# Kernel tuning notes

Hardware: AMD Instinct MI355X
Metric: run time of the kernel (lower is better)

Reference implementation:

```python
import jax, jax.numpy as jnp
import numpy as np

B, S, H = 8, 1024, 1024
NH, HD = 16, 64
MBANK, TOPK = 128, 16
NLAYERS, FF = 12, 4096
EPS = 1e-5


def _ln(x, w, b):
    m = x.mean(-1, keepdims=True)
    v = ((x - m) ** 2).mean(-1, keepdims=True)
    return (x - m) / jnp.sqrt(v + EPS) * w + b


def _split_heads(x):  # [B,S,H] -> [B,NH,S,HD]
    return x.reshape(B, S, NH, HD).transpose(0, 2, 1, 3)


def _sdpa(q, k, v):  # inputs [B,NH,S,HD]
    scores = jnp.einsum('bhqd,bhkd->bhqk', q, k) / jnp.sqrt(jnp.float32(HD))
    attn = jax.nn.softmax(scores, axis=-1)
    o = jnp.einsum('bhqk,bhkd->bhqd', attn, v)
    return o.transpose(0, 2, 1, 3).reshape(B, S, H)


def setup_inputs() -> dict:
    key = jax.random.key(0)
    ks = jax.random.split(key, 24)
    n = lambda k, shp, s=0.02: jax.random.normal(k, shp, jnp.float32) * s
    return {
        'hidden_states': jax.random.normal(ks[0], (B, S, H), jnp.float32),
        'ln1_w': jnp.ones((H,), jnp.float32), 'ln1_b': jnp.zeros((H,), jnp.float32),
        'ln2_w': jnp.ones((H,), jnp.float32), 'ln2_b': jnp.zeros((H,), jnp.float32),
        'rec_wq': n(ks[1], (H, H)), 'rec_wk': n(ks[2], (H, H)),
        'rec_wv': n(ks[3], (H, H)), 'rec_wo': n(ks[4], (H, H)),
        'rec_ad_w1': n(ks[5], (H // 4, H)), 'rec_ad_w2': n(ks[6], (H, H // 4)),
        'mem_bank': n(ks[7], (MBANK, H)),
        'alloc_w': n(ks[8], (MBANK, H)), 'alloc_b': jnp.zeros((MBANK,), jnp.float32),
        'retr_w': n(ks[9], (MBANK, H)), 'retr_b': jnp.zeros((MBANK,), jnp.float32),
        'upd_w': n(ks[10], (H, H)), 'upd_b': jnp.zeros((H,), jnp.float32),
        'mem_scales': jnp.full((NLAYERS,), 0.1, jnp.float32),
        'attn_in_w': n(ks[11], (3 * H, H)), 'attn_in_b': jnp.zeros((3 * H,), jnp.float32),
        'attn_out_w': n(ks[12], (H, H)), 'attn_out_b': jnp.zeros((H,), jnp.float32),
        'mlp_w1': n(ks[13], (FF, H)), 'mlp_b1': jnp.zeros((FF,), jnp.float32),
        'mlp_w2': n(ks[14], (H, FF)), 'mlp_b2': jnp.zeros((H,), jnp.float32),
        'layer_idx': 4,
    }


def reference(hidden_states, ln1_w, ln1_b, ln2_w, ln2_b,
              rec_wq, rec_wk, rec_wv, rec_wo, rec_ad_w1, rec_ad_w2,
              mem_bank, alloc_w, alloc_b, retr_w, retr_b, upd_w, upd_b, mem_scales,
              attn_in_w, attn_in_b, attn_out_w, attn_out_b,
              mlp_w1, mlp_b1, mlp_w2, mlp_b2, layer_idx):
    residual = hidden_states
    h = _ln(hidden_states, ln1_w, ln1_b)

    # --- CrossLayerParameterRecycler (layer_idx % 4 == 0 and > 0 -> recycle) ---
    if layer_idx % 4 == 0 and layer_idx > 0:
        q = _split_heads(h @ rec_wq.T)
        k = _split_heads(h @ rec_wk.T)
        v = _split_heads(h @ rec_wv.T)
        base_out = _sdpa(q, k, v) @ rec_wo.T
        h = jax.nn.relu(base_out @ rec_ad_w1.T) @ rec_ad_w2.T

    # --- CrossLayerMemoryManager ---
    pooled = h.mean(axis=1)                                  # [B,H]
    alloc_weights = jax.nn.softmax(pooled @ alloc_w.T + alloc_b, axis=-1)   # [B,MBANK]
    retr_weights = jax.nn.softmax(pooled @ retr_w.T + retr_b, axis=-1)
    retrieved = retr_weights @ mem_bank                      # [B,H]
    h = h + retrieved[:, None, :] * mem_scales[layer_idx]
    update_signals = jax.nn.sigmoid(h.mean(axis=1) @ upd_w.T + upd_b)       # [B,H]
    _, top_idx = jax.lax.top_k(alloc_weights, TOPK)          # [B,TOPK]

    # sequential per-batch scatter (later batches overwrite earlier, as in torch loop)
    def _write(mb, be):
        idx, sig = be
        return mb.at[idx].set(jnp.broadcast_to(sig, (TOPK, H))), None
    new_mem_bank, _ = jax.lax.scan(_write, mem_bank, (top_idx, update_signals))

    # --- self attention (nn.MultiheadAttention, batch_first) ---
    qkv = h @ attn_in_w.T + attn_in_b                        # [B,S,3H]
    q, k, v = jnp.split(qkv, 3, axis=-1)
    attn_out = _sdpa(_split_heads(q), _split_heads(k), _split_heads(v))
    attn_out = attn_out @ attn_out_w.T + attn_out_b
    h = residual + attn_out

    # --- MLP block ---
    residual2 = h
    h = _ln(h, ln2_w, ln2_b)
    h = jax.nn.gelu(h @ mlp_w1.T + mlp_b1, approximate=False) @ mlp_w2.T + mlp_b2
    out = residual2 + h
    return out, new_mem_bank
```

## Files before the change

### kernel.cpp

```cpp
#include <hip/hip_runtime.h>
#include <hip/hip_bf16.h>
#include <math.h>
#include <stdint.h>


#define BB 8
#define SS 1024
#define HH 1024
#define NHEAD 16
#define HD 64
#define MBANK 128
#define TOPK_N 16
#define FF_DIM 4096
#define MROWS (BB * SS)
#define NB_ELEM (8ull*1024*1024)

typedef __bf16 bf16x8 __attribute__((ext_vector_type(8)));
typedef __bf16 bf16x4 __attribute__((ext_vector_type(4)));
typedef float f32x4 __attribute__((ext_vector_type(4)));

#define SCALE_LOG2E 0.18033688011112042f

__device__ __forceinline__ unsigned short f2b(float x) {
  unsigned u = __float_as_uint(x);
  unsigned r = (u + 0x7FFFu + ((u >> 16) & 1u)) >> 16;
  return (unsigned short)r;
}
__device__ __forceinline__ float b2f(unsigned short u) {
  return __uint_as_float((unsigned)u << 16);
}

__device__ __forceinline__ float hmax4(f32x4 v) {
  return fmaxf(fmaxf(v[0], v[1]), fmaxf(v[2], v[3]));
}

__device__ __forceinline__ void load16_lds(const void* g, void* lds_base, int lane) {
#if __has_builtin(__builtin_amdgcn_global_load_lds)
  typedef const __attribute__((address_space(1))) unsigned int guint;
  typedef __attribute__((address_space(3))) unsigned int luint;
  __builtin_amdgcn_global_load_lds((guint*)(uintptr_t)g,
                                   (luint*)(unsigned long long)(unsigned int)(uintptr_t)lds_base,
                                   16, 0, 0);
#else
  *(uint4*)((char*)lds_base + lane * 16) = *(const uint4*)g;
#endif
}

__device__ __forceinline__ float gelu_exact(float x) {
  return 0.5f * x * (1.f + erff(x * 0.70710678118654752440f));
}


__global__ __launch_bounds__(256) void cast_split(const float* __restrict__ s,
                                                  unsigned short* __restrict__ hi,
                                                  unsigned short* __restrict__ lo, int n4) {
  int i = blockIdx.x * 256 + threadIdx.x;
  if (i < n4) {
    float4 v = ((const float4*)s)[i];
    ushort4 h, l;
    h.x = f2b(v.x); l.x = f2b(v.x - b2f(h.x));
    h.y = f2b(v.y); l.y = f2b(v.y - b2f(h.y));
    h.z = f2b(v.z); l.z = f2b(v.z - b2f(h.z));
    h.w = f2b(v.w); l.w = f2b(v.w - b2f(h.w));
    ((ushort4*)hi)[i] = h;
    ((ushort4*)lo)[i] = l;
  }
}

__global__ __launch_bounds__(256) void ln3(const float* __restrict__ x,
                                           const float* __restrict__ w,
                                           const float* __restrict__ b,
                                           unsigned short* __restrict__ yh,
                                           unsigned short* __restrict__ yl) {
  int row = blockIdx.x;
  const float* xr = x + (size_t)row * HH;
  int t = threadIdx.x;
  float v[4];
  float s = 0.f, ss = 0.f;
#pragma unroll
  for (int i = 0; i < 4; i++) {
    v[i] = xr[t + i * 256];
    s += v[i];
    ss += v[i] * v[i];
  }
  __shared__ float rs[8], rss[8];
  for (int o = 32; o > 0; o >>= 1) {
    s += __shfl_down(s, o, 64);
    ss += __shfl_down(ss, o, 64);
  }
  int wid = t >> 6, lane = t & 63;
  if (lane == 0) { rs[wid] = s; rss[wid] = ss; }
  __syncthreads();
  if (t == 0) {
    float S = rs[0] + rs[1] + rs[2] + rs[3];
    float SSum = rss[0] + rss[1] + rss[2] + rss[3];
    float m = S * (1.f / HH);
    float var = SSum * (1.f / HH) - m * m;
    rs[4] = m;
    rs[5] = rsqrtf(var + 1e-5f);
  }
  __syncthreads();
  float m = rs[4], inv = rs[5];
#pragma unroll
  for (int i = 0; i < 4; i++) {
    int c = t + i * 256;
    float y = (v[i] - m) * inv * w[c] + b[c];
    unsigned short h = f2b(y);
    yh[(size_t)row * HH + c] = h;
    yl[(size_t)row * HH + c] = f2b(y - b2f(h));
  }
}

template <int ACT, int MODE>
__global__ __launch_bounds__(256) void gemm3(const unsigned short* __restrict__ Ah,
                                             const unsigned short* __restrict__ Al, int lda,
                                             const unsigned short* __restrict__ Wh,
                                             const unsigned short* __restrict__ Wl, int ldw,
                                             unsigned short* __restrict__ Oh,
                                             unsigned short* __restrict__ Ol,
                                             float* __restrict__ outF,
                                             int ldo, int K) {
  __shared__ unsigned short Ash[2][128 * 32];
  __shared__ unsigned short Asl[2][128 * 32];
  __shared__ unsigned short Bsh[2][128 * 32];
  __shared__ unsigned short Bsl[2][128 * 32];
  int n0 = blockIdx.x * 128, m0 = blockIdx.y * 128;
  int t = threadIdx.x, w = t >> 6, L = t & 63, quad = L >> 4, l16 = L & 15;
  int wm = w & 1, wn = w >> 1;
  const f32x4 vzero = {0.f, 0.f, 0.f, 0.f};
  f32x4 acc[4][4];
#pragma unroll
  for (int i = 0; i < 4; i++)
#pragma unroll
    for (int j = 0; j < 4; j++) acc[i][j] = vzero;
  int srow = L >> 2;
  int scol = ((L & 3) ^ ((L >> 3) & 3)) * 8;
  int rsw = (l16 >> 1) & 3;

  auto stage = [&](int buf, int k0) {
#pragma unroll
    for (int c = 0; c < 2; c++) {
      int r = (c * 4 + w) * 16 + srow;
      size_t aoff = (size_t)(m0 + r) * lda + k0 + scol;
      size_t boff = (size_t)(n0 + r) * ldw + k0 + scol;
      load16_lds(Ah + aoff, &Ash[buf][(c * 4 + w) * 512], L);
      load16_lds(Al + aoff, &Asl[buf][(c * 4 + w) * 512], L);
      load16_lds(Wh + boff, &Bsh[buf][(c * 4 + w) * 512], L);
      load16_lds(Wl + boff, &Bsl[buf][(c * 4 + w) * 512], L);
    }
  };
  auto compute = [&](int buf) {
    bf16x8 afh[4], afl[4], bfh[4], bfl[4];
#pragma unroll
    for (int i = 0; i < 4; i++) {
      int off = (wm * 64 + i * 16 + l16) * 32 + (quad ^ rsw) * 8;
      afh[i] = *(const bf16x8*)&Ash[buf][off];
      afl[i] = *(const bf16x8*)&Asl[buf][off];
    }
#pragma unroll
    for (int j = 0; j < 4; j++) {
      int off = (wn * 64 + j * 16 + l16) * 32 + (quad ^ rsw) * 8;
      bfh[j] = *(const bf16x8*)&Bsh[buf][off];
      bfl[j] = *(const bf16x8*)&Bsl[buf][off];
    }
#pragma unroll
    for (int i = 0; i < 4; i++)
#pragma unroll
      for (int j = 0; j < 4; j++) {
        acc[i][j] = __builtin_amdgcn_mfma_f32_16x16x32_bf16(afh[i], bfh[j], acc[i][j], 0, 0, 0);
        acc[i][j] = __builtin_amdgcn_mfma_f32_16x16x32_bf16(afh[i], bfl[j], acc[i][j], 0, 0, 0);
        acc[i][j] = __builtin_amdgcn_mfma_f32_16x16x32_bf16(afl[i], bfh[j], acc[i][j], 0, 0, 0);
      }
  };

  stage(0, 0);
  __syncthreads();
  for (int k0 = 0; k0 < K; k0 += 64) {
    stage(1, k0 + 32);
    compute(0);
    __syncthreads();
    if (k0 + 64 < K) stage(0, k0 + 64);
    compute(1);
    __syncthreads();
  }
#pragma unroll
  for (int i = 0; i < 4; i++) {
    int mb = m0 + wm * 64 + i * 16 + quad * 4;
#pragma unroll
    for (int j = 0; j < 4; j++) {
      int n = n0 + wn * 64 + j * 16 + l16;
      if (MODE == 1) {
        ushort4 sh, sl;
        float vv[4];
#pragma unroll
        for (int r = 0; r < 4; r++) {
          float v = acc[i][j][r];
          if (ACT == 1) v = fmaxf(v, 0.f);
          vv[r] = v;
        }
        sh.x = f2b(vv[0]); sl.x = f2b(vv[0] - b2f(sh.x));
        sh.y = f2b(vv[1]); sl.y = f2b(vv[1] - b2f(sh.y));
        sh.z = f2b(vv[2]); sl.z = f2b(vv[2] - b2f(sh.z));
        sh.w = f2b(vv[3]); sl.w = f2b(vv[3] - b2f(sh.w));
        *(ushort4*)&Oh[(size_t)n * ldo + mb] = sh;
        *(ushort4*)&Ol[(size_t)n * ldo + mb] = sl;
      } else {
#pragma unroll
        for (int r = 0; r < 4; r++) {
          float v = acc[i][j][r];
          if (ACT == 1) v = fmaxf(v, 0.f);
          size_t off = (size_t)(mb + r) * ldo + n;
          if (MODE == 0) {
            unsigned short h = f2b(v);
            Oh[off] = h;
            Ol[off] = f2b(v - b2f(h));
          } else {
            outF[off] = v;
          }
        }
      }
    }
  }
}

__global__ __launch_bounds__(256) void sdpa3(const unsigned short* __restrict__ Qh,
                                             const unsigned short* __restrict__ Ql,
                                             const unsigned short* __restrict__ Kh,
                                             const unsigned short* __restrict__ Kl,
                                             const unsigned short* __restrict__ Vth,
                                             const unsigned short* __restrict__ Vtl,
                                             unsigned short* __restrict__ Oh,
                                             unsigned short* __restrict__ Ol) {
  __shared__ unsigned short Ksh[64 * 64];
  __shared__ unsigned short Ksl[64 * 64];
  __shared__ unsigned short Vsh[64 * 64];
  __shared__ unsigned short Vsl[64 * 64];
  int wg = (int)blockIdx.x;
  int swz = (wg & 7) * 256 + (wg >> 3);
  int qt = swz & 15, h = (swz >> 4) & 15, b = swz >> 8;
  int t = threadIdx.x, w = t >> 6, L = t & 63, quad = L >> 4, l16 = L & 15;
  int q0 = qt * 64;
  const f32x4 vzero = {0.f, 0.f, 0.f, 0.f};
  bf16x8 qfh[2], qfl[2];
  {
    size_t qrow = (size_t)(b * SS + q0 + w * 16 + l16);
#pragma unroll
    for (int kh = 0; kh < 2; kh++) {
      size_t off = qrow * HH + h * 64 + kh * 32 + quad * 8;
      qfh[kh] = *(const bf16x8*)&Qh[off];
      qfl[kh] = *(const bf16x8*)&Ql[off];
    }
  }
  float mprev = -1e30f, lsum = 0.f;
  f32x4 oacc[4];
#pragma unroll
  for (int jd = 0; jd < 4; jd++) oacc[jd] = vzero;
  int srow = L >> 3;
  int scolV = ((L & 7) ^ srow) * 8;
  int rbase = ((l16 & 12) << 1) | (l16 & 3);
  int keyK = (l16 & 3) | (((l16 >> 2) & 1) << 2);
  int k7 = l16 & 7;
  for (int k0 = 0; k0 < SS; k0 += 64) {
    __syncthreads();
#pragma unroll
    for (int c = 0; c < 2; c++) {
      int rr = (c * 4 + w) * 8 + srow;
      int scolK = ((L & 7) ^ ((srow & 3) | (((c * 4 + w) & 1) << 2))) * 8;
      size_t koff = (size_t)(b * SS + k0 + rr) * HH + h * 64 + scolK;
      size_t voff = (size_t)(h * 64 + rr) * MROWS + b * SS + k0 + scolV;
      load16_lds(Kh + koff, &Ksh[(c * 4 + w) * 512], L);
      load16_lds(Kl + koff, &Ksl[(c * 4 + w) * 512], L);
      load16_lds(Vth + voff, &Vsh[(c * 4 + w) * 512], L);
      load16_lds(Vtl + voff, &Vsl[(c * 4 + w) * 512], L);
    }
    __syncthreads();
    f32x4 sacc[4];
#pragma unroll
    for (int jn = 0; jn < 4; jn++) sacc[jn] = vzero;
#pragma unroll
    for (int jn = 0; jn < 4; jn++) {
      int rowp = rbase + (jn & 1) * 4 + (jn >> 1) * 32;
#pragma unroll
      for (int kh = 0; kh < 2; kh++) {
        int off = rowp * 64 + (((kh * 4 + quad) ^ keyK) << 3);
        bf16x8 kfh = *(const bf16x8*)&Ksh[off];
        bf16x8 kfl = *(const bf16x8*)&Ksl[off];
        sacc[jn] = __builtin_amdgcn_mfma_f32_16x16x32_bf16(kfh, qfh[kh], sacc[jn], 0, 0, 0);
        sacc[jn] = __builtin_amdgcn_mfma_f32_16x16x32_bf16(kfl, qfh[kh], sacc[jn], 0, 0, 0);
        sacc[jn] = __builtin_amdgcn_mfma_f32_16x16x32_bf16(kfh, qfl[kh], sacc[jn], 0, 0, 0);
      }
    }
    float mt = fmaxf(fmaxf(hmax4(sacc[0]), hmax4(sacc[1])),
                     fmaxf(hmax4(sacc[2]), hmax4(sacc[3])));
    mt = fmaxf(mt, __shfl_xor(mt, 16, 64));
    mt = fmaxf(mt, __shfl_xor(mt, 32, 64));
    float m2 = fmaxf(mprev, mt * SCALE_LOG2E);
    float rs = 0.f;
    bf16x8 pah[2], pal[2];
#pragma unroll
    for (int jn = 0; jn < 4; jn++) {
      int kh = jn >> 1, half = (jn & 1) * 4;
#pragma unroll
      for (int r = 0; r < 4; r++) {
        float p = exp2f(fmaf(sacc[jn][r], SCALE_LOG2E, -m2));
        rs += p;
        __bf16 ph = (__bf16)p;
        pah[kh][half + r] = ph;
        pal[kh][half + r] = (__bf16)(p - (float)ph);
      }
    }
    rs += __shfl_xor(rs, 16, 64);
    rs += __shfl_xor(rs, 32, 64);
    if (__any(m2 != mprev)) {
      float alpha = exp2f(mprev - m2);
      lsum = lsum * alpha + rs;
      float ar[4];
#pragma unroll
      for (int r = 0; r < 4; r++) ar[r] = __shfl(alpha, quad * 4 + r, 16);
#pragma unroll
      for (int jd = 0; jd < 4; jd++)
#pragma unroll
        for (int r = 0; r < 4; r++) oacc[jd][r] *= ar[r];
    } else {
      lsum += rs;
    }
    mprev = m2;
#pragma unroll
    for (int jd = 0; jd < 4; jd++)
#pragma unroll
      for (int kh = 0; kh < 2; kh++) {
        int off = (jd * 16 + l16) * 64 + ((kh * 4 + quad) ^ k7) * 8;
        bf16x8 vfh = *(const bf16x8*)&Vsh[off];
        bf16x8 vfl = *(const bf16x8*)&Vsl[off];
        oacc[jd] = __builtin_amdgcn_mfma_f32_16x16x32_bf16(pah[kh], vfh, oacc[jd], 0, 0, 0);
        oacc[jd] = __builtin_amdgcn_mfma_f32_16x16x32_bf16(pah[kh], vfl, oacc[jd], 0, 0, 0);
        oacc[jd] = __builtin_amdgcn_mfma_f32_16x16x32_bf16(pal[kh], vfh, oacc[jd], 0, 0, 0);
      }
  }
  float inv = 1.f / lsum;
  float invr[4];
#pragma unroll
  for (int r = 0; r < 4; r++) invr[r] = __shfl(inv, quad * 4 + r, 16);
#pragma unroll
  for (int r = 0; r < 4; r++) {
    size_t row = (size_t)(b * SS + q0 + w * 16 + quad * 4 + r);
#pragma unroll
    for (int jd = 0; jd < 4; jd++) {
      float v = oacc[jd][r] * invr[r];
      unsigned short hh = f2b(v);
      size_t off = row * HH + h * 64 + jd * 16 + l16;
      Oh[off] = hh;
      Ol[off] = f2b(v - b2f(hh));
    }
  }
}


__global__ __launch_bounds__(256) void meanpool_kernel(const float* __restrict__ Hb,
                                                       float* __restrict__ P) {
  int cb = blockIdx.x;
  int b = blockIdx.y;
  int t = threadIdx.x;
  int c = (t & 63) + cb * 64;
  int part = t >> 6;
  float s = 0.f;
  const float* p = Hb + ((size_t)b * SS + part * 256) * HH + c;
  for (int j = 0; j < 256; j++) s += p[(size_t)j * HH];
  __shared__ float red[4][64];
  red[part][t & 63] = s;
  __syncthreads();
  if (t < 64) {
    float tot = red[0][t] + red[1][t] + red[2][t] + red[3][t];
    P[b * HH + cb * 64 + t] = tot * (1.f / SS);
  }
}

__global__ __launch_bounds__(256) void memlogits_kernel(const float* __restrict__ P,
                                                        const float* __restrict__ AW,
                                                        const float* __restrict__ ABias,
                                                        const float* __restrict__ RW,
                                                        const float* __restrict__ RBias,
                                                        float* __restrict__ LA,
                                                        float* __restrict__ LR) {
  int m = blockIdx.x, b = blockIdx.y;
  int t = threadIdx.x;
  const float* pr = P + b * HH;
  const float* aw = AW + (size_t)m * HH;
  const float* rw = RW + (size_t)m * HH;
  float sa = 0.f, sr = 0.f;
  for (int i = t; i < HH; i += 256) {
    float pv = pr[i];
    sa = fmaf(pv, aw[i], sa);
    sr = fmaf(pv, rw[i], sr);
  }
  for (int o = 32; o > 0; o >>= 1) {
    sa += __shfl_down(sa, o, 64);
    sr += __shfl_down(sr, o, 64);
  }
  __shared__ float ra[4], rr[4];
  if ((t & 63) == 0) { ra[t >> 6] = sa; rr[t >> 6] = sr; }
  __syncthreads();
  if (t == 0) {
    LA[b * MBANK + m] = ra[0] + ra[1] + ra[2] + ra[3] + ABias[m];
    LR[b * MBANK + m] = rr[0] + rr[1] + rr[2] + rr[3] + RBias[m];
  }
}

__global__ __launch_bounds__(256) void retrieve_kernel(const float* __restrict__ LA,
                                                       const float* __restrict__ LR,
                                                       const float* __restrict__ MB,
                                                       float* __restrict__ RET,
                                                       int* __restrict__ ISTOP) {
  int b = blockIdx.x;
  int t = threadIdx.x;
  __shared__ float rw[MBANK];
  __shared__ float la[MBANK];
  if (t < MBANK) {
    la[t] = LA[b * MBANK + t];
    rw[t] = LR[b * MBANK + t];
  }
  __syncthreads();
  if (t == 0) {
    float mx = -1e30f;
    for (int i = 0; i < MBANK; i++) mx = fmaxf(mx, rw[i]);
    float s = 0.f;
    for (int i = 0; i < MBANK; i++) {
      float e = __expf(rw[i] - mx);
      rw[i] = e;
      s += e;
    }
    float inv = 1.f / s;
    for (int i = 0; i < MBANK; i++) rw[i] *= inv;
  }
  __syncthreads();
  if (t < MBANK) {
    float mine = la[t];
    int rank = 0;
    for (int i = 0; i < MBANK; i++) {
      float o = la[i];
      if (o > mine || (o == mine && i < t)) rank++;
    }
    ISTOP[b * MBANK + t] = (rank < TOPK_N) ? 1 : 0;
  }
  for (int c = t; c < HH; c += 256) {
    float s = 0.f;
    for (int m = 0; m < MBANK; m++) s = fmaf(rw[m], MB[(size_t)m * HH + c], s);
    RET[b * HH + c] = s;
  }
}

__global__ __launch_bounds__(256) void addmem_kernel(float* __restrict__ Hb,
                                                     const float* __restrict__ RET,
                                                     const float* __restrict__ scales,
                                                     const int* __restrict__ lidx) {
  float sc = scales[lidx[0]];
  size_t i = (size_t)blockIdx.x * 256 + threadIdx.x;
  int c = (int)(i & 1023);
  int b = (int)(i >> 20);
  Hb[i] = fmaf(RET[b * HH + c], sc, Hb[i]);
}

__global__ __launch_bounds__(256) void upd_kernel(const float* __restrict__ P2,
                                                  const float* __restrict__ UW,
                                                  const float* __restrict__ UB,
                                                  float* __restrict__ UPD) {
  int n = blockIdx.x, b = blockIdx.y;
  int t = threadIdx.x;
  const float* pr = P2 + b * HH;
  const float* wr = UW + (size_t)n * HH;
  float s = 0.f;
  for (int i = t; i < HH; i += 256) s = fmaf(pr[i], wr[i], s);
  for (int o = 32; o > 0; o >>= 1) s += __shfl_down(s, o, 64);
  __shared__ float red[4];
  if ((t & 63) == 0) red[t >> 6] = s;
  __syncthreads();
  if (t == 0) {
    float tot = red[0] + red[1] + red[2] + red[3] + UB[n];
    UPD[b * HH + n] = 1.f / (1.f + __expf(-tot));
  }
}

__global__ __launch_bounds__(256) void membank_kernel(const float* __restrict__ MB,
                                                      const int* __restrict__ ISTOP,
                                                      const float* __restrict__ UPD,
                                                      float* __restrict__ OUT) {
  int row = blockIdx.x;
  int col = blockIdx.y * 256 + threadIdx.x;
  int w = -1;
  for (int b = 0; b < BB; b++)
    if (ISTOP[b * MBANK + row]) w = b;
  float v = (w >= 0) ? UPD[w * HH + col] : MB[(size_t)row * HH + col];
  OUT[(size_t)row * HH + col] = v;
}


__global__ __launch_bounds__(256) void ln_bf(const float* __restrict__ x,
                                             const float* __restrict__ w,
                                             const float* __restrict__ b,
                                             unsigned short* __restrict__ y) {
  int row = blockIdx.x;
  const float* xr = x + (size_t)row * HH;
  unsigned short* yr = y + (size_t)row * HH;
  int t = threadIdx.x;
  float v[4];
  float s = 0.f, ss = 0.f;
#pragma unroll
  for (int i = 0; i < 4; i++) {
    v[i] = xr[t + i * 256];
    s += v[i];
    ss += v[i] * v[i];
  }
  __shared__ float rs[8], rss[8];
  for (int o = 32; o > 0; o >>= 1) {
    s += __shfl_down(s, o, 64);
    ss += __shfl_down(ss, o, 64);
  }
  int wid = t >> 6, lane = t & 63;
  if (lane == 0) { rs[wid] = s; rss[wid] = ss; }
  __syncthreads();
  if (t == 0) {
    float S = rs[0] + rs[1] + rs[2] + rs[3];
    float SSum = rss[0] + rss[1] + rss[2] + rss[3];
    float m = S * (1.f / HH);
    float var = SSum * (1.f / HH) - m * m;
    rs[4] = m;
    rs[5] = rsqrtf(var + 1e-5f);
  }
  __syncthreads();
  float m = rs[4], inv = rs[5];
#pragma unroll
  for (int i = 0; i < 4; i++) {
    int c = t + i * 256;
    yr[c] = f2b((v[i] - m) * inv * w[c] + b[c]);
  }
}

__global__ __launch_bounds__(256) void castf2b(const float* __restrict__ s,
                                               unsigned short* __restrict__ d, int n4) {
  int i = blockIdx.x * 256 + threadIdx.x;
  if (i < n4) {
    float4 v = ((const float4*)s)[i];
    ushort4 o;
    o.x = f2b(v.x); o.y = f2b(v.y); o.z = f2b(v.z); o.w = f2b(v.w);
    ((ushort4*)d)[i] = o;
  }
}

template <int ACT, int MODE>
__global__ __launch_bounds__(256) void gemm_bf(const unsigned short* __restrict__ A, int lda,
                                               const unsigned short* __restrict__ W, int ldw,
                                               const float* __restrict__ bias,
                                               const float* __restrict__ resid,
                                               float* __restrict__ outF,
                                               unsigned short* __restrict__ outB,
                                               int ldo, int K) {
  __shared__ unsigned short As[2][128 * 32];
  __shared__ unsigned short Bs[2][128 * 32];
  int n0 = blockIdx.x * 128, m0 = blockIdx.y * 128;
  int t = threadIdx.x, w = t >> 6, L = t & 63, quad = L >> 4, l16 = L & 15;
  int wm = w & 1, wn = w >> 1;
  const f32x4 vzero = {0.f, 0.f, 0.f, 0.f};
  f32x4 acc[4][4];
#pragma unroll
  for (int i = 0; i < 4; i++)
#pragma unroll
    for (int j = 0; j < 4; j++) acc[i][j] = vzero;
  int srow = L >> 2;
  int scol = ((L & 3) ^ ((L >> 3) & 3)) * 8;
  int rsw = (l16 >> 1) & 3;

  auto stage = [&](int buf, int k0) {
#pragma unroll
    for (int c = 0; c < 2; c++) {
      int r = (c * 4 + w) * 16 + srow;
      load16_lds(A + (size_t)(m0 + r) * lda + k0 + scol, &As[buf][(c * 4 + w) * 512], L);
      load16_lds(W + (size_t)(n0 + r) * ldw + k0 + scol, &Bs[buf][(c * 4 + w) * 512], L);
    }
  };
  auto compute = [&](int buf) {
    bf16x8 af[4], bfr[4];
#pragma unroll
    for (int i = 0; i < 4; i++)
      af[i] = *(const bf16x8*)&As[buf][(wm * 64 + i * 16 + l16) * 32 + (quad ^ rsw) * 8];
#pragma unroll
    for (int j = 0; j < 4; j++)
      bfr[j] = *(const bf16x8*)&Bs[buf][(wn * 64 + j * 16 + l16) * 32 + (quad ^ rsw) * 8];
#pragma unroll
    for (int i = 0; i < 4; i++)
#pragma unroll
      for (int j = 0; j < 4; j++)
        acc[i][j] = __builtin_amdgcn_mfma_f32_16x16x32_bf16(af[i], bfr[j], acc[i][j], 0, 0, 0);
  };

  stage(0, 0);
  __syncthreads();
  for (int k0 = 0; k0 < K; k0 += 64) {
    stage(1, k0 + 32);
    compute(0);
    __syncthreads();
    if (k0 + 64 < K) stage(0, k0 + 64);
    compute(1);
    __syncthreads();
  }
#pragma unroll
  for (int i = 0; i < 4; i++) {
    int mb = m0 + wm * 64 + i * 16 + quad * 4;
#pragma unroll
    for (int j = 0; j < 4; j++) {
      int n = n0 + wn * 64 + j * 16 + l16;
      float bv = bias ? bias[n] : 0.f;
      if (MODE == 2) {
        ushort4 st;
        float v0 = acc[i][j][0] + bv, v1 = acc[i][j][1] + bv;
        float v2 = acc[i][j][2] + bv, v3 = acc[i][j][3] + bv;
        if (ACT == 1) { v0 = fmaxf(v0, 0.f); v1 = fmaxf(v1, 0.f); v2 = fmaxf(v2, 0.f); v3 = fmaxf(v3, 0.f); }
        if (ACT == 2) { v0 = gelu_exact(v0); v1 = gelu_exact(v1); v2 = gelu_exact(v2); v3 = gelu_exact(v3); }
        st.x = f2b(v0); st.y = f2b(v1); st.z = f2b(v2); st.w = f2b(v3);
        *(ushort4*)&outB[(size_t)n * ldo + mb] = st;
      } else {
#pragma unroll
        for (int r = 0; r < 4; r++) {
          float v = acc[i][j][r] + bv;
          if (ACT == 1) v = fmaxf(v, 0.f);
          if (ACT == 2) v = gelu_exact(v);
          size_t off = (size_t)(mb + r) * ldo + n;
          if (MODE == 1) outB[off] = f2b(v);
          else if (MODE == 3) outF[off] += v;
          else if (MODE == 4) outF[off] = v + resid[off];
        }
      }
    }
  }
}

__global__ __launch_bounds__(256) void sdpa_bf(const unsigned short* __restrict__ Q,
                                               const unsigned short* __restrict__ Kb,
                                               const unsigned short* __restrict__ Vt,
                                               unsigned short* __restrict__ O) {
  __shared__ unsigned short Ks[64 * 64];
  __shared__ unsigned short Vs[64 * 64];
  int wg = (int)blockIdx.x;
  int swz = (wg & 7) * 256 + (wg >> 3);
  int qt = swz & 15, h = (swz >> 4) & 15, b = swz >> 8;
  int t = threadIdx.x, w = t >> 6, L = t & 63, quad = L >> 4, l16 = L & 15;
  int q0 = qt * 64;
  const f32x4 vzero = {0.f, 0.f, 0.f, 0.f};
  bf16x8 qf[2];
  {
    size_t qrow = (size_t)(b * SS + q0 + w * 16 + l16);
#pragma unroll
    for (int kh = 0; kh < 2; kh++)
      qf[kh] = *(const bf16x8*)&Q[qrow * HH + h * 64 + kh * 32 + quad * 8];
  }
  float mprev = -1e30f, lsum = 0.f;
  f32x4 oacc[4];
#pragma unroll
  for (int jd = 0; jd < 4; jd++) oacc[jd] = vzero;
  int srow = L >> 3;
  int scolV = ((L & 7) ^ srow) * 8;
  int rbase = ((l16 & 12) << 1) | (l16 & 3);
  int keyK = (l16 & 3) | (((l16 >> 2) & 1) << 2);
  int k7 = l16 & 7;
  for (int k0 = 0; k0 < SS; k0 += 64) {
    __syncthreads();
#pragma unroll
    for (int c = 0; c < 2; c++) {
      int rr = (c * 4 + w) * 8 + srow;
      int scolK = ((L & 7) ^ ((srow & 3) | (((c * 4 + w) & 1) << 2))) * 8;
      load16_lds(Kb + (size_t)(b * SS + k0 + rr) * HH + h * 64 + scolK, &Ks[(c * 4 + w) * 512], L);
      load16_lds(Vt + (size_t)(h * 64 + rr) * MROWS + b * SS + k0 + scolV, &Vs[(c * 4 + w) * 512], L);
    }
    __syncthreads();
    f32x4 sacc[4];
#pragma unroll
    for (int jn = 0; jn < 4; jn++) sacc[jn] = vzero;
#pragma unroll
    for (int jn = 0; jn < 4; jn++) {
      int rowp = rbase + (jn & 1) * 4 + (jn >> 1) * 32;
#pragma unroll
      for (int kh = 0; kh < 2; kh++) {
        bf16x8 kf = *(const bf16x8*)&Ks[rowp * 64 + (((kh * 4 + quad) ^ keyK) << 3)];
        sacc[jn] = __builtin_amdgcn_mfma_f32_16x16x32_bf16(kf, qf[kh], sacc[jn], 0, 0, 0);
      }
    }
    float mt = fmaxf(fmaxf(hmax4(sacc[0]), hmax4(sacc[1])),
                     fmaxf(hmax4(sacc[2]), hmax4(sacc[3])));
    mt = fmaxf(mt, __shfl_xor(mt, 16, 64));
    mt = fmaxf(mt, __shfl_xor(mt, 32, 64));
    float m2 = fmaxf(mprev, mt * SCALE_LOG2E);
    float rs = 0.f;
    bf16x8 pa[2];
#pragma unroll
    for (int jn = 0; jn < 4; jn++) {
      int kh = jn >> 1, half = (jn & 1) * 4;
#pragma unroll
      for (int r = 0; r < 4; r++) {
        float p = exp2f(fmaf(sacc[jn][r], SCALE_LOG2E, -m2));
        rs += p;
        pa[kh][half + r] = (__bf16)p;
      }
    }
    rs += __shfl_xor(rs, 16, 64);
    rs += __shfl_xor(rs, 32, 64);
    if (__any(m2 != mprev)) {
      float alpha = exp2f(mprev - m2);
      lsum = lsum * alpha + rs;
      float ar[4];
#pragma unroll
      for (int r = 0; r < 4; r++) ar[r] = __shfl(alpha, quad * 4 + r, 16);
#pragma unroll
      for (int jd = 0; jd < 4; jd++)
#pragma unroll
        for (int r = 0; r < 4; r++) oacc[jd][r] *= ar[r];
    } else {
      lsum += rs;
    }
    mprev = m2;
#pragma unroll
    for (int jd = 0; jd < 4; jd++)
#pragma unroll
      for (int kh = 0; kh < 2; kh++) {
        bf16x8 vf = *(const bf16x8*)&Vs[(jd * 16 + l16) * 64 + ((kh * 4 + quad) ^ k7) * 8];
        oacc[jd] = __builtin_amdgcn_mfma_f32_16x16x32_bf16(pa[kh], vf, oacc[jd], 0, 0, 0);
      }
  }
  float inv = 1.f / lsum;
  float invr[4];
#pragma unroll
  for (int r = 0; r < 4; r++) invr[r] = __shfl(inv, quad * 4 + r, 16);
#pragma unroll
  for (int r = 0; r < 4; r++) {
    size_t row = (size_t)(b * SS + q0 + w * 16 + quad * 4 + r);
#pragma unroll
    for (int jd = 0; jd < 4; jd++)
      O[row * HH + h * 64 + jd * 16 + l16] = f2b(oacc[jd][r] * invr[r]);
  }
}

extern "C" void kernel_launch(void* const* d_in, const int* in_sizes, int n_in,
                              void* d_out, int out_size, void* d_ws, size_t ws_size,
                              hipStream_t stream) {
  const float* x = (const float*)d_in[0];
  const float* ln1_w = (const float*)d_in[1];
  const float* ln1_b = (const float*)d_in[2];
  const float* ln2_w = (const float*)d_in[3];
  const float* ln2_b = (const float*)d_in[4];
  const float* rec_wq = (const float*)d_in[5];
  const float* rec_wk = (const float*)d_in[6];
  const float* rec_wv = (const float*)d_in[7];
  const float* rec_wo = (const float*)d_in[8];
  const float* rec_ad_w1 = (const float*)d_in[9];
  const float* rec_ad_w2 = (const float*)d_in[10];
  const float* mem_bank = (const float*)d_in[11];
  const float* alloc_w = (const float*)d_in[12];
  const float* alloc_b = (const float*)d_in[13];
  const float* retr_w = (const float*)d_in[14];
  const float* retr_b = (const float*)d_in[15];
  const float* upd_w = (const float*)d_in[16];
  const float* upd_b = (const float*)d_in[17];
  const float* mem_scales = (const float*)d_in[18];
  const float* attn_in_w = (const float*)d_in[19];
  const float* attn_in_b = (const float*)d_in[20];
  const float* attn_out_w = (const float*)d_in[21];
  const float* attn_out_b = (const float*)d_in[22];
  const float* mlp_w1 = (const float*)d_in[23];
  const float* mlp_b1 = (const float*)d_in[24];
  const float* mlp_w2 = (const float*)d_in[25];
  const float* mlp_b2 = (const float*)d_in[26];
  const int* layer_idx = (const int*)d_in[27];

  float* out = (float*)d_out;
  float* out_mb = out + NB_ELEM;

  const size_t U = NB_ELEM;
  unsigned short* W16 = (unsigned short*)d_ws;
  unsigned short* U0 = W16;
  unsigned short* U1 = W16 + U;
  unsigned short* U2 = W16 + 2 * U;
  unsigned short* U3 = W16 + 3 * U;
  unsigned short* U4 = W16 + 4 * U;
  unsigned short* U5 = W16 + 5 * U;
  unsigned short* wsh = W16 + 6 * U;
  unsigned short* wsl = wsh + 1048576;
  float* small = (float*)(wsl + 1048576);
  float* pooled = small;
  float* pooled2 = small + 8192;
  float* logitsA = small + 16384;
  float* logitsR = small + 17408;
  float* retrieved = small + 18432;
  float* updsig = small + 26624;
  int* istop = (int*)(small + 34816);
  unsigned short* D0 = (unsigned short*)out;
  unsigned short* D1 = D0 + U;
  unsigned short* ain_bf = U5;
  unsigned short* aout_bf = U5 + 3 * 1048576;

  dim3 blk(256);
  dim3 gG(8, 64);
  dim3 gG256(2, 64);
  dim3 gS1(2048);
  const int EW_GRID = (int)(NB_ELEM / 256);

  ln3<<<MROWS, blk, 0, stream>>>(x, ln1_w, ln1_b, U0, U1);
  cast_split<<<1024, blk, 0, stream>>>(rec_wq, wsh, wsl, 262144);
  gemm3<0, 0><<<gG, blk, 0, stream>>>(U0, U1, HH, wsh, wsl, HH, U2, U3, nullptr, HH, HH);
  cast_split<<<1024, blk, 0, stream>>>(rec_wk, wsh, wsl, 262144);
  gemm3<0, 0><<<gG, blk, 0, stream>>>(U0, U1, HH, wsh, wsl, HH, U4, U5, nullptr, HH, HH);
  cast_split<<<1024, blk, 0, stream>>>(rec_wv, wsh, wsl, 262144);
  gemm3<0, 1><<<gG, blk, 0, stream>>>(U0, U1, HH, wsh, wsl, HH, D0, D1, nullptr, MROWS, HH);
  sdpa3<<<gS1, blk, 0, stream>>>(U2, U3, U4, U5, D0, D1, U0, U1);
  cast_split<<<1024, blk, 0, stream>>>(rec_wo, wsh, wsl, 262144);
  gemm3<0, 0><<<gG, blk, 0, stream>>>(U0, U1, HH, wsh, wsl, HH, U2, U3, nullptr, HH, HH);
  cast_split<<<256, blk, 0, stream>>>(rec_ad_w1, wsh, wsl, 65536);
  gemm3<1, 0><<<gG256, blk, 0, stream>>>(U2, U3, HH, wsh, wsl, HH, U4, U4 + 2097152, nullptr, 256, HH);
  cast_split<<<256, blk, 0, stream>>>(rec_ad_w2, wsh, wsl, 65536);
  gemm3<0, 2><<<gG, blk, 0, stream>>>(U4, U4 + 2097152, 256, wsh, wsl, 256, nullptr, nullptr, out, HH, 256);
  meanpool_kernel<<<dim3(HH / 64, BB), blk, 0, stream>>>(out, pooled);
  memlogits_kernel<<<dim3(MBANK, BB), blk, 0, stream>>>(pooled, alloc_w, alloc_b, retr_w, retr_b, logitsA, logitsR);
  retrieve_kernel<<<BB, blk, 0, stream>>>(logitsA, logitsR, mem_bank, retrieved, istop);
  addmem_kernel<<<EW_GRID, blk, 0, stream>>>(out, retrieved, mem_scales, layer_idx);
  meanpool_kernel<<<dim3(HH / 64, BB), blk, 0, stream>>>(out, pooled2);
  upd_kernel<<<dim3(HH, BB), blk, 0, stream>>>(pooled2, upd_w, upd_b, updsig);
  membank_kernel<<<dim3(MBANK, HH / 256), blk, 0, stream>>>(mem_bank, istop, updsig, out_mb);
  castf2b<<<8192, blk, 0, stream>>>(out, U0, 2097152);
  castf2b<<<3072, blk, 0, stream>>>(attn_in_w, ain_bf, 786432);
  castf2b<<<1024, blk, 0, stream>>>(attn_out_w, aout_bf, 262144);
  gemm_bf<0, 1><<<gG, blk, 0, stream>>>(U0, HH, ain_bf, HH, attn_in_b, nullptr, nullptr, U1, HH, HH);
  gemm_bf<0, 1><<<gG, blk, 0, stream>>>(U0, HH, ain_bf + (size_t)HH * HH, HH, attn_in_b + HH, nullptr, nullptr, U2, HH, HH);
  gemm_bf<0, 2><<<gG, blk, 0, stream>>>(U0, HH, ain_bf + 2ull * HH * HH, HH, attn_in_b + 2 * HH, nullptr, nullptr, U3, MROWS, HH);
  sdpa_bf<<<gS1, blk, 0, stream>>>(U1, U2, U3, U4);
  gemm_bf<0, 4><<<gG, blk, 0, stream>>>(U4, HH, aout_bf, HH, attn_out_b, x, out, nullptr, HH, HH);
  ln_bf<<<MROWS, blk, 0, stream>>>(out, ln2_w, ln2_b, U1);
  {
    unsigned short* w1b = U0;
    unsigned short* w2b = U0 + 4 * 1048576;
    unsigned short* h2 = U2;
    castf2b<<<4096, blk, 0, stream>>>(mlp_w1, w1b, 1048576);
    castf2b<<<4096, blk, 0, stream>>>(mlp_w2, w2b, 1048576);
    gemm_bf<2, 1><<<dim3(32, 64), blk, 0, stream>>>(U1, HH, w1b, HH, mlp_b1, nullptr, nullptr, h2, FF_DIM, HH);
    gemm_bf<0, 3><<<gG, blk, 0, stream>>>(h2, FF_DIM, w2b, FF_DIM, mlp_b2, nullptr, out, nullptr, HH, FF_DIM);
  }
}
```

Before: 1.126 ms.

## Fuse memory-add into update and casts, merge cast launches, single-buffer gemm3

Removes the separate add-memory pass over the hidden states and the second mean-pool by folding the retrieved*scale term into the update GEMV and into the bf16 cast of the hidden states. Merges several weight-cast launches into combined kernels to cut launch count. It also changes gemm3 from double-buffered LDS staging to a single buffer with two barriers per 32-wide K step. That halves gemm3's LDS footprint but removes the load/compute overlap. The memory-add fusion relies on linearity of the mean, since pooled + ret*scale equals the mean of h + ret*scale.

```diff
diff --git a/kernel.cpp b/kernel.cpp
--- a/kernel.cpp
+++ b/kernel.cpp
@@ -16,7 +16,6 @@
 #define NB_ELEM (8ull*1024*1024)
 
 typedef __bf16 bf16x8 __attribute__((ext_vector_type(8)));
-typedef __bf16 bf16x4 __attribute__((ext_vector_type(4)));
 typedef float f32x4 __attribute__((ext_vector_type(4)));
 
 #define SCALE_LOG2E 0.18033688011112042f
@@ -67,6 +66,30 @@
   }
 }
 
+__global__ __launch_bounds__(256) void cast_split2(const float* __restrict__ s1,
+                                                   unsigned short* __restrict__ h1,
+                                                   unsigned short* __restrict__ l1, int n1,
+                                                   const float* __restrict__ s2,
+                                                   unsigned short* __restrict__ h2,
+                                                   unsigned short* __restrict__ l2, int n2) {
+  int i = blockIdx.x * 256 + threadIdx.x;
+  const float* s;
+  unsigned short* hh;
+  unsigned short* ll;
+  int j;
+  if (i < n1) { s = s1; hh = h1; ll = l1; j = i; }
+  else if (i < n1 + n2) { s = s2; hh = h2; ll = l2; j = i - n1; }
+  else return;
+  float4 v = ((const float4*)s)[j];
+  ushort4 h, l;
+  h.x = f2b(v.x); l.x = f2b(v.x - b2f(h.x));
+  h.y = f2b(v.y); l.y = f2b(v.y - b2f(h.y));
+  h.z = f2b(v.z); l.z = f2b(v.z - b2f(h.z));
+  h.w = f2b(v.w); l.w = f2b(v.w - b2f(h.w));
+  ((ushort4*)hh)[j] = h;
+  ((ushort4*)ll)[j] = l;
+}
+
 __global__ __launch_bounds__(256) void ln3(const float* __restrict__ x,
                                            const float* __restrict__ w,
                                            const float* __restrict__ b,
@@ -120,10 +143,10 @@
                                              unsigned short* __restrict__ Ol,
                                              float* __restrict__ outF,
                                              int ldo, int K) {
-  __shared__ unsigned short Ash[2][128 * 32];
-  __shared__ unsigned short Asl[2][128 * 32];
-  __shared__ unsigned short Bsh[2][128 * 32];
-  __shared__ unsigned short Bsl[2][128 * 32];
+  __shared__ unsigned short Ash[128 * 32];
+  __shared__ unsigned short Asl[128 * 32];
+  __shared__ unsigned short Bsh[128 * 32];
+  __shared__ unsigned short Bsl[128 * 32];
   int n0 = blockIdx.x * 128, m0 = blockIdx.y * 128;
   int t = threadIdx.x, w = t >> 6, L = t & 63, quad = L >> 4, l16 = L & 15;
   int wm = w & 1, wn = w >> 1;
@@ -136,32 +159,31 @@
   int srow = L >> 2;
   int scol = ((L & 3) ^ ((L >> 3) & 3)) * 8;
   int rsw = (l16 >> 1) & 3;
-
-  auto stage = [&](int buf, int k0) {
+  for (int k0 = 0; k0 < K; k0 += 32) {
+    __syncthreads();
 #pragma unroll
     for (int c = 0; c < 2; c++) {
       int r = (c * 4 + w) * 16 + srow;
       size_t aoff = (size_t)(m0 + r) * lda + k0 + scol;
       size_t boff = (size_t)(n0 + r) * ldw + k0 + scol;
-      load16_lds(Ah + aoff, &Ash[buf][(c * 4 + w) * 512], L);
-      load16_lds(Al + aoff, &Asl[buf][(c * 4 + w) * 512], L);
-      load16_lds(Wh + boff, &Bsh[buf][(c * 4 + w) * 512], L);
-      load16_lds(Wl + boff, &Bsl[buf][(c * 4 + w) * 512], L);
-    }
-  };
-  auto compute = [&](int buf) {
+      load16_lds(Ah + aoff, &Ash[(c * 4 + w) * 512], L);
+      load16_lds(Al + aoff, &Asl[(c * 4 + w) * 512], L);
+      load16_lds(Wh + boff, &Bsh[(c * 4 + w) * 512], L);
+      load16_lds(Wl + boff, &Bsl[(c * 4 + w) * 512], L);
+    }
+    __syncthreads();
     bf16x8 afh[4], afl[4], bfh[4], bfl[4];
 #pragma unroll
     for (int i = 0; i < 4; i++) {
       int off = (wm * 64 + i * 16 + l16) * 32 + (quad ^ rsw) * 8;
-      afh[i] = *(const bf16x8*)&Ash[buf][off];
-      afl[i] = *(const bf16x8*)&Asl[buf][off];
+      afh[i] = *(const bf16x8*)&Ash[off];
+      afl[i] = *(const bf16x8*)&Asl[off];
     }
 #pragma unroll
     for (int j = 0; j < 4; j++) {
       int off = (wn * 64 + j * 16 + l16) * 32 + (quad ^ rsw) * 8;
-      bfh[j] = *(const bf16x8*)&Bsh[buf][off];
-      bfl[j] = *(const bf16x8*)&Bsl[buf][off];
+      bfh[j] = *(const bf16x8*)&Bsh[off];
+      bfl[j] = *(const bf16x8*)&Bsl[off];
     }
 #pragma unroll
     for (int i = 0; i < 4; i++)
@@ -171,17 +193,6 @@
         acc[i][j] = __builtin_amdgcn_mfma_f32_16x16x32_bf16(afh[i], bfl[j], acc[i][j], 0, 0, 0);
         acc[i][j] = __builtin_amdgcn_mfma_f32_16x16x32_bf16(afl[i], bfh[j], acc[i][j], 0, 0, 0);
       }
-  };
-
-  stage(0, 0);
-  __syncthreads();
-  for (int k0 = 0; k0 < K; k0 += 64) {
-    stage(1, k0 + 32);
-    compute(0);
-    __syncthreads();
-    if (k0 + 64 < K) stage(0, k0 + 64);
-    compute(1);
-    __syncthreads();
   }
 #pragma unroll
   for (int i = 0; i < 4; i++) {
@@ -449,27 +460,24 @@
   }
 }
 
-__global__ __launch_bounds__(256) void addmem_kernel(float* __restrict__ Hb,
-                                                     const float* __restrict__ RET,
-                                                     const float* __restrict__ scales,
-                                                     const int* __restrict__ lidx) {
-  float sc = scales[lidx[0]];
-  size_t i = (size_t)blockIdx.x * 256 + threadIdx.x;
-  int c = (int)(i & 1023);
-  int b = (int)(i >> 20);
-  Hb[i] = fmaf(RET[b * HH + c], sc, Hb[i]);
-}
-
-__global__ __launch_bounds__(256) void upd_kernel(const float* __restrict__ P2,
+__global__ __launch_bounds__(256) void upd_kernel(const float* __restrict__ P,
+                                                  const float* __restrict__ RETR,
+                                                  const float* __restrict__ scales,
+                                                  const int* __restrict__ lidx,
                                                   const float* __restrict__ UW,
                                                   const float* __restrict__ UB,
                                                   float* __restrict__ UPD) {
   int n = blockIdx.x, b = blockIdx.y;
   int t = threadIdx.x;
-  const float* pr = P2 + b * HH;
+  float sc = scales[lidx[0]];
+  const float* pr = P + b * HH;
+  const float* rr2 = RETR + b * HH;
   const float* wr = UW + (size_t)n * HH;
   float s = 0.f;
-  for (int i = t; i < HH; i += 256) s = fmaf(pr[i], wr[i], s);
+  for (int i = t; i < HH; i += 256) {
+    float pv = fmaf(rr2[i], sc, pr[i]);
+    s = fmaf(pv, wr[i], s);
+  }
   for (int o = 32; o > 0; o >>= 1) s += __shfl_down(s, o, 64);
   __shared__ float red[4];
   if ((t & 63) == 0) red[t >> 6] = s;
@@ -535,15 +543,59 @@
   }
 }
 
-__global__ __launch_bounds__(256) void castf2b(const float* __restrict__ s,
-                                               unsigned short* __restrict__ d, int n4) {
+__global__ __launch_bounds__(256) void cast_attn_fused(const float* __restrict__ hs,
+                                                       const float* __restrict__ ret,
+                                                       const float* __restrict__ scales,
+                                                       const int* __restrict__ lidx,
+                                                       const float* __restrict__ ain_w,
+                                                       const float* __restrict__ aout_w,
+                                                       unsigned short* __restrict__ h_bf,
+                                                       unsigned short* __restrict__ ain_bf,
+                                                       unsigned short* __restrict__ aout_bf) {
   int i = blockIdx.x * 256 + threadIdx.x;
-  if (i < n4) {
-    float4 v = ((const float4*)s)[i];
+  if (i < 2097152) {
+    float sc = scales[lidx[0]];
+    float4 v = ((const float4*)hs)[i];
+    int e = i << 2;
+    int b = e >> 20;
+    int c = e & 1023;
+    float4 r4 = *(const float4*)&ret[b * HH + c];
+    ushort4 o;
+    o.x = f2b(fmaf(r4.x, sc, v.x));
+    o.y = f2b(fmaf(r4.y, sc, v.y));
+    o.z = f2b(fmaf(r4.z, sc, v.z));
+    o.w = f2b(fmaf(r4.w, sc, v.w));
+    ((ushort4*)h_bf)[i] = o;
+  } else if (i < 2097152 + 786432) {
+    int j = i - 2097152;
+    float4 v = ((const float4*)ain_w)[j];
     ushort4 o;
     o.x = f2b(v.x); o.y = f2b(v.y); o.z = f2b(v.z); o.w = f2b(v.w);
-    ((ushort4*)d)[i] = o;
-  }
+    ((ushort4*)ain_bf)[j] = o;
+  } else if (i < 2097152 + 786432 + 262144) {
+    int j = i - 2097152 - 786432;
+    float4 v = ((const float4*)aout_w)[j];
+    ushort4 o;
+    o.x = f2b(v.x); o.y = f2b(v.y); o.z = f2b(v.z); o.w = f2b(v.w);
+    ((ushort4*)aout_bf)[j] = o;
+  }
+}
+
+__global__ __launch_bounds__(256) void castf2b2(const float* __restrict__ s1,
+                                                unsigned short* __restrict__ d1, int n1,
+                                                const float* __restrict__ s2,
+                                                unsigned short* __restrict__ d2, int n2) {
+  int i = blockIdx.x * 256 + threadIdx.x;
+  const float* s;
+  unsigned short* d;
+  int j;
+  if (i < n1) { s = s1; d = d1; j = i; }
+  else if (i < n1 + n2) { s = s2; d = d2; j = i - n1; }
+  else return;
+  float4 v = ((const float4*)s)[j];
+  ushort4 o;
+  o.x = f2b(v.x); o.y = f2b(v.y); o.z = f2b(v.z); o.w = f2b(v.w);
+  ((ushort4*)d)[j] = o;
 }
 
 template <int ACT, int MODE>
@@ -784,7 +836,6 @@
   unsigned short* wsl = wsh + 1048576;
   float* small = (float*)(wsl + 1048576);
   float* pooled = small;
-  float* pooled2 = small + 8192;
   float* logitsA = small + 16384;
   float* logitsR = small + 17408;
   float* retrieved = small + 18432;
@@ -792,6 +843,12 @@
   int* istop = (int*)(small + 34816);
   unsigned short* D0 = (unsigned short*)out;
   unsigned short* D1 = D0 + U;
+  unsigned short* wkh = D0;
+  unsigned short* wkl = D0 + 1048576;
+  unsigned short* a1h = U0;
+  unsigned short* a1l = U0 + 262144;
+  unsigned short* a2h = U0 + 524288;
+  unsigned short* a2l = U0 + 786432;
   unsigned short* ain_bf = U5;
   unsigned short* aout_bf = U5 + 3 * 1048576;
 
@@ -799,32 +856,26 @@
   dim3 gG(8, 64);
   dim3 gG256(2, 64);
   dim3 gS1(2048);
-  const int EW_GRID = (int)(NB_ELEM / 256);
 
   ln3<<<MROWS, blk, 0, stream>>>(x, ln1_w, ln1_b, U0, U1);
-  cast_split<<<1024, blk, 0, stream>>>(rec_wq, wsh, wsl, 262144);
+  cast_split2<<<2048, blk, 0, stream>>>(rec_wq, wsh, wsl, 262144, rec_wk, wkh, wkl, 262144);
   gemm3<0, 0><<<gG, blk, 0, stream>>>(U0, U1, HH, wsh, wsl, HH, U2, U3, nullptr, HH, HH);
-  cast_split<<<1024, blk, 0, stream>>>(rec_wk, wsh, wsl, 262144);
-  gemm3<0, 0><<<gG, blk, 0, stream>>>(U0, U1, HH, wsh, wsl, HH, U4, U5, nullptr, HH, HH);
+  gemm3<0, 0><<<gG, blk, 0, stream>>>(U0, U1, HH, wkh, wkl, HH, U4, U5, nullptr, HH, HH);
   cast_split<<<1024, blk, 0, stream>>>(rec_wv, wsh, wsl, 262144);
   gemm3<0, 1><<<gG, blk, 0, stream>>>(U0, U1, HH, wsh, wsl, HH, D0, D1, nullptr, MROWS, HH);
   sdpa3<<<gS1, blk, 0, stream>>>(U2, U3, U4, U5, D0, D1, U0, U1);
   cast_split<<<1024, blk, 0, stream>>>(rec_wo, wsh, wsl, 262144);
   gemm3<0, 0><<<gG, blk, 0, stream>>>(U0, U1, HH, wsh, wsl, HH, U2, U3, nullptr, HH, HH);
-  cast_split<<<256, blk, 0, stream>>>(rec_ad_w1, wsh, wsl, 65536);
-  gemm3<1, 0><<<gG256, blk, 0, stream>>>(U2, U3, HH, wsh, wsl, HH, U4, U4 + 2097152, nullptr, 256, HH);
-  cast_split<<<256, blk, 0, stream>>>(rec_ad_w2, wsh, wsl, 65536);
-  gemm3<0, 2><<<gG, blk, 0, stream>>>(U4, U4 + 2097152, 256, wsh, wsl, 256, nullptr, nullptr, out, HH, 256);
+  cast_split2<<<512, blk, 0, stream>>>(rec_ad_w1, a1h, a1l, 65536, rec_ad_w2, a2h, a2l, 65536);
+  gemm3<1, 0><<<gG256, blk, 0, stream>>>(U2, U3, HH, a1h, a1l, HH, U4, U4 + 2097152, nullptr, 256, HH);
+  gemm3<0, 2><<<gG, blk, 0, stream>>>(U4, U4 + 2097152, 256, a2h, a2l, 256, nullptr, nullptr, out, HH, 256);
   meanpool_kernel<<<dim3(HH / 64, BB), blk, 0, stream>>>(out, pooled);
   memlogits_kernel<<<dim3(MBANK, BB), blk, 0, stream>>>(pooled, alloc_w, alloc_b, retr_w, retr_b, logitsA, logitsR);
   retrieve_kernel<<<BB, blk, 0, stream>>>(logitsA, logitsR, mem_bank, retrieved, istop);
-  addmem_kernel<<<EW_GRID, blk, 0, stream>>>(out, retrieved, mem_scales, layer_idx);
-  meanpool_kernel<<<dim3(HH / 64, BB), blk, 0, stream>>>(out, pooled2);
-  upd_kernel<<<dim3(HH, BB), blk, 0, stream>>>(pooled2, upd_w, upd_b, updsig);
+  upd_kernel<<<dim3(HH, BB), blk, 0, stream>>>(pooled, retrieved, mem_scales, layer_idx, upd_w, upd_b, updsig);
   membank_kernel<<<dim3(MBANK, HH / 256), blk, 0, stream>>>(mem_bank, istop, updsig, out_mb);
-  castf2b<<<8192, blk, 0, stream>>>(out, U0, 2097152);
-  castf2b<<<3072, blk, 0, stream>>>(attn_in_w, ain_bf, 786432);
-  castf2b<<<1024, blk, 0, stream>>>(attn_out_w, aout_bf, 262144);
+  cast_attn_fused<<<12288, blk, 0, stream>>>(out, retrieved, mem_scales, layer_idx,
+                                             attn_in_w, attn_out_w, U0, ain_bf, aout_bf);
   gemm_bf<0, 1><<<gG, blk, 0, stream>>>(U0, HH, ain_bf, HH, attn_in_b, nullptr, nullptr, U1, HH, HH);
   gemm_bf<0, 1><<<gG, blk, 0, stream>>>(U0, HH, ain_bf + (size_t)HH * HH, HH, attn_in_b + HH, nullptr, nullptr, U2, HH, HH);
   gemm_bf<0, 2><<<gG, blk, 0, stream>>>(U0, HH, ain_bf + 2ull * HH * HH, HH, attn_in_b + 2 * HH, nullptr, nullptr, U3, MROWS, HH);
@@ -835,8 +886,7 @@
     unsigned short* w1b = U0;
     unsigned short* w2b = U0 + 4 * 1048576;
     unsigned short* h2 = U2;
-    castf2b<<<4096, blk, 0, stream>>>(mlp_w1, w1b, 1048576);
-    castf2b<<<4096, blk, 0, stream>>>(mlp_w2, w2b, 1048576);
+    castf2b2<<<8192, blk, 0, stream>>>(mlp_w1, w1b, 1048576, mlp_w2, w2b, 1048576);
     gemm_bf<2, 1><<<dim3(32, 64), blk, 0, stream>>>(U1, HH, w1b, HH, mlp_b1, nullptr, nullptr, h2, FF_DIM, HH);
     gemm_bf<0, 3><<<gG, blk, 0, stream>>>(h2, FF_DIM, w2b, FF_DIM, mlp_b2, nullptr, out, nullptr, HH, FF_DIM);
   }
```

Measured after the change: 1.114 ms (median of 2 runs). Within noise of the previous version (-1.0%).
